# Kernel tuning notes

Measured on AMD Instinct MI355X. Metric: run time of the kernel, lower is better.

The kernel has to match this reference:

```python
import jax, jax.numpy as jnp
import numpy as np

C = 256
H = 4  # hard-coded head count in SA_Layer reshapes
EPS = 1e-5


def _bn(x, gamma, beta):
    # training-mode BatchNorm1d over (batch, length) per channel; x: [b,c,n]
    m = jnp.mean(x, axis=(0, 2), keepdims=True)
    v = jnp.var(x, axis=(0, 2), keepdims=True)
    return gamma[None, :, None] * (x - m) * jax.lax.rsqrt(v + EPS) + beta[None, :, None]


def _conv1(w, x, b=None):
    # 1x1 Conv1d == per-point matmul; w: [o,c], x: [b,c,n]
    y = jnp.einsum('oc,bcn->bon', w, x)
    return y if b is None else y + b[None, :, None]


def _sa_layer(x, xyz_emb, qk_w, v_w, v_b, t_w, t_b, bn_g, bn_b):
    b, c, n = x.shape
    h = x + xyz_emb                      # [b,c,n]
    q = _conv1(qk_w, h)                  # [b,c,n]  (q and k share weights)
    # quirky reshape: permute to [b,n,c] then view as [b,H,n,c//H]
    x_q = jnp.transpose(q, (0, 2, 1)).reshape(b, H, n, c // H)
    x_k = q.reshape(b, H, c // H, n)     # standard channel head split
    x_v = _conv1(v_w, h, v_b).reshape(b, H, c // H, n)
    energy = jnp.matmul(x_q, x_k)        # [b,H,n,n]
    att = jax.nn.softmax(energy, axis=-1)
    att = jax.nn.softmax(att, axis=-2)   # dual softmax
    x_r = jnp.matmul(x_v, att).reshape(b, c, n)
    x_r = jax.nn.relu(_bn(_conv1(t_w, x - x_r, t_b), bn_g, bn_b))
    return x + x_r


def setup_inputs() -> dict:
    key = jax.random.key(0)
    ks = jax.random.split(key, 16)
    B, N = 4, 2048
    s = 1.0 / np.sqrt(C)
    inp = {
        'x': jax.random.normal(ks[0], (B, C, N), jnp.float32),
        'xyz': jax.random.normal(ks[1], (B, N, 3), jnp.float32),
        'conv1_w': jax.random.normal(ks[2], (C, C), jnp.float32) * s,
        'pos_w': jax.random.normal(ks[3], (C, 3), jnp.float32) * 0.5,
        'pos_b': jax.random.normal(ks[4], (C,), jnp.float32) * 0.02,
        'bn1_g': jnp.ones((C,), jnp.float32),
        'bn1_b': jnp.zeros((C,), jnp.float32),
        'qk_w': jax.random.normal(ks[5], (4, C, C), jnp.float32) * s,
        'v_w': jax.random.normal(ks[6], (4, C, C), jnp.float32) * s,
        'v_b': jax.random.normal(ks[7], (4, C), jnp.float32) * 0.02,
        't_w': jax.random.normal(ks[8], (4, C, C), jnp.float32) * s,
        't_b': jax.random.normal(ks[9], (4, C), jnp.float32) * 0.02,
        'bn_g': jnp.ones((4, C), jnp.float32),
        'bn_b': jnp.zeros((4, C), jnp.float32),
    }
    return inp


def reference(x, xyz, conv1_w, pos_w, pos_b, bn1_g, bn1_b,
              qk_w, v_w, v_b, t_w, t_b, bn_g, bn_b):
    # xyz: [B,N,3] -> permute -> pos_xyz (1x1 conv)
    xyz_emb = jnp.einsum('oi,bni->bon', pos_w, xyz) + pos_b[None, :, None]  # [b,C,n]
    h = jax.nn.relu(_bn(_conv1(conv1_w, x), bn1_g, bn1_b))
    outs = []
    for i in range(4):
        h = _sa_layer(h, xyz_emb, qk_w[i], v_w[i], v_b[i],
                      t_w[i], t_b[i], bn_g[i], bn_b[i])
        outs.append(h)
    return jnp.concatenate(outs, axis=1)  # [b, 4*C, n]
```

## Files before the change

### kernel.cpp

```cpp
#include <hip/hip_runtime.h>
#include <math.h>

#define Bsz 4
#define Cch 256
#define Npt 2048
#define Hh  4
#define NL  4
#define BN_CNT (Bsz * Npt)
#define EPSV 1e-5f
#define NROW (16 * Npt)
#define L2E 1.44269504f
#define NIC 4

typedef _Float16 f16x8 __attribute__((ext_vector_type(8)));
typedef _Float16 f16x4 __attribute__((ext_vector_type(4)));
typedef float    f32x4 __attribute__((ext_vector_type(4)));

__device__ __forceinline__ float fexp2(float x) { return __builtin_amdgcn_exp2f(x); }

__device__ __forceinline__ void gld16(const _Float16* g, _Float16* l) {
    __builtin_amdgcn_global_load_lds(
        (const __attribute__((address_space(1))) unsigned int*)g,
        (__attribute__((address_space(3))) unsigned int*)l, 16, 0, 0);
}

__global__ void k_xyz_emb(const float* __restrict__ xyz, const float* __restrict__ pw,
                          const float* __restrict__ pb, float* __restrict__ emb) {
    int idx = blockIdx.x * 256 + threadIdx.x;
    int n = idx & (Npt - 1);
    int c = (idx >> 11) & (Cch - 1);
    int b = idx >> 19;
    const float* xz = xyz + (b * Npt + n) * 3;
    emb[idx] = pw[c * 3 + 0] * xz[0] + pw[c * 3 + 1] * xz[1] + pw[c * 3 + 2] * xz[2] + pb[c];
}

__global__ void k_castw(const float* __restrict__ c1w, const float* __restrict__ qkw,
                        const float* __restrict__ vw, const float* __restrict__ tw,
                        _Float16* __restrict__ o, float* __restrict__ bnacc) {
    int i = blockIdx.x * 256 + threadIdx.x;
    if (i < 5 * 512) bnacc[i] = 0.f;
    const float* src; int off;
    if (i < 65536)            { src = c1w; off = i; }
    else if (i < 327680)      { src = qkw; off = i - 65536; }
    else if (i < 589824)      { src = vw;  off = i - 327680; }
    else                      { src = tw;  off = i - 589824; }
    o[i] = (_Float16)src[off];
}

__global__ __launch_bounds__(256) void k_fuse_t(const float* __restrict__ in,
        _Float16* __restrict__ XT) {
    __shared__ _Float16 Tt[64][72];
    const int b = blockIdx.z, c0 = blockIdx.y * 64, n0 = blockIdx.x * 64;
    const int t = threadIdx.x;
    const int cl = t >> 2, ns = (t & 3) * 16;
    const float* ip = in + ((size_t)(b * Cch + c0 + cl) * Npt) + n0 + ns;
    #pragma unroll
    for (int g = 0; g < 4; ++g) {
        float4 v = *(const float4*)(ip + g * 4);
        Tt[ns + g * 4 + 0][cl] = (_Float16)v.x;
        Tt[ns + g * 4 + 1][cl] = (_Float16)v.y;
        Tt[ns + g * 4 + 2][cl] = (_Float16)v.z;
        Tt[ns + g * 4 + 3][cl] = (_Float16)v.w;
    }
    __syncthreads();
    int nl = t >> 2, cs = (t & 3) * 16;
    _Float16* op = XT + ((size_t)(b * Npt + n0 + nl) * Cch) + c0 + cs;
    #pragma unroll
    for (int g = 0; g < 4; ++g)
        *(f16x4*)(op + g * 4) = *(f16x4*)&Tt[nl][cs + g * 4];
}

__global__ __launch_bounds__(256) void k_gemm_mfma(const _Float16* __restrict__ Wb,
        const _Float16* __restrict__ XT, const float* __restrict__ bias,
        float* __restrict__ Yf, float* __restrict__ bnacc) {
    __shared__ float EpF[64][68];
    const int b = blockIdx.z, o0 = blockIdx.y * 64, n0 = blockIdx.x * 64;
    const int tid = threadIdx.x, w = tid >> 6, quad = (tid >> 4) & 3, tx = tid & 15;
    const _Float16* Arow = Wb + (o0 + w * 16 + tx) * Cch + quad * 8;
    const _Float16* Brow = XT + ((size_t)(b * Npt + n0 + tx) * Cch) + quad * 8;
    f32x4 acc[4];
    #pragma unroll
    for (int s = 0; s < 4; ++s) acc[s] = (f32x4){0.f, 0.f, 0.f, 0.f};
    for (int k0 = 0; k0 < Cch; k0 += 32) {
        f16x8 a = *(const f16x8*)(Arow + k0);
        #pragma unroll
        for (int s = 0; s < 4; ++s) {
            f16x8 bb = *(const f16x8*)(Brow + s * 16 * Cch + k0);
            acc[s] = __builtin_amdgcn_mfma_f32_16x16x32_f16(a, bb, acc[s], 0, 0, 0);
        }
    }
    float bv[4];
    {
        int ob = o0 + w * 16 + quad * 4;
        if (bias) { bv[0] = bias[ob]; bv[1] = bias[ob + 1]; bv[2] = bias[ob + 2]; bv[3] = bias[ob + 3]; }
        else bv[0] = bv[1] = bv[2] = bv[3] = 0.f;
    }
    #pragma unroll
    for (int s = 0; s < 4; ++s) {
        int ol = w * 16 + quad * 4, nl = s * 16 + tx;
        EpF[ol + 0][nl] = acc[s][0] + bv[0];
        EpF[ol + 1][nl] = acc[s][1] + bv[1];
        EpF[ol + 2][nl] = acc[s][2] + bv[2];
        EpF[ol + 3][nl] = acc[s][3] + bv[3];
    }
    __syncthreads();
    int row = tid >> 2, seg = (tid & 3) * 16;
    float* yp = Yf + ((size_t)(b * Cch + o0 + row) * Npt) + n0 + seg;
    float s1 = 0.f, s2 = 0.f;
    #pragma unroll
    for (int g = 0; g < 4; ++g) {
        float4 v = *(float4*)&EpF[row][seg + g * 4];
        *(float4*)(yp + g * 4) = v;
        s1 += v.x + v.y + v.z + v.w;
        s2 += v.x * v.x + v.y * v.y + v.z * v.z + v.w * v.w;
    }
    s1 += __shfl_xor(s1, 1); s2 += __shfl_xor(s2, 1);
    s1 += __shfl_xor(s1, 2); s2 += __shfl_xor(s2, 2);
    if ((tid & 3) == 0) {
        atomicAdd(&bnacc[o0 + row], s1);
        atomicAdd(&bnacc[256 + o0 + row], s2);
    }
}

__global__ __launch_bounds__(256) void k_gemm_qkv(const _Float16* __restrict__ Wqk,
        const _Float16* __restrict__ Wv, const _Float16* __restrict__ XT,
        const float* __restrict__ vbias, _Float16* __restrict__ Vb,
        _Float16* __restrict__ Qg, _Float16* __restrict__ Kt) {
    __shared__ _Float16 EpB[64][72];
    const int b = blockIdx.z, y = blockIdx.y, n0 = blockIdx.x * 64;
    const int isV = (y >= 4);
    const int o0 = (isV ? (y - 4) : y) * 64;
    const _Float16* Wb = isV ? Wv : Wqk;
    const int tid = threadIdx.x, w = tid >> 6, quad = (tid >> 4) & 3, tx = tid & 15;
    const _Float16* Arow = Wb + (o0 + w * 16 + tx) * Cch + quad * 8;
    const _Float16* Brow = XT + ((size_t)(b * Npt + n0 + tx) * Cch) + quad * 8;
    f32x4 acc[4];
    #pragma unroll
    for (int s = 0; s < 4; ++s) acc[s] = (f32x4){0.f, 0.f, 0.f, 0.f};
    for (int k0 = 0; k0 < Cch; k0 += 32) {
        f16x8 a = *(const f16x8*)(Arow + k0);
        #pragma unroll
        for (int s = 0; s < 4; ++s) {
            f16x8 bb = *(const f16x8*)(Brow + s * 16 * Cch + k0);
            acc[s] = __builtin_amdgcn_mfma_f32_16x16x32_f16(a, bb, acc[s], 0, 0, 0);
        }
    }
    if (!isV) {
        const int cch = (w << 1) + (quad >> 1);
        const int hof = (quad & 1) * 4;
        #pragma unroll
        for (int s = 0; s < 4; ++s) {
            int ng = n0 + s * 16 + tx;
            f16x4 pk;
            pk[0] = (_Float16)acc[s][0]; pk[1] = (_Float16)acc[s][1];
            pk[2] = (_Float16)acc[s][2]; pk[3] = (_Float16)acc[s][3];
            int rK = ng & 63, jt = ng >> 6;
            size_t ka = ((size_t)((b * Hh + (o0 >> 6)) * 32 + jt) << 12)
                      + rK * 64 + ((cch ^ (rK & 7)) * 8) + hof;
            *(f16x4*)&Kt[ka] = pk;
            int iQ = ((ng & 511) << 2) + (o0 >> 6);
            int rQ = iQ & 63, it = iQ >> 6;
            size_t qa = ((size_t)((b * Hh + (ng >> 9)) * 32 + it) << 12)
                      + rQ * 64 + ((cch ^ (rQ & 7)) * 8) + hof;
            *(f16x4*)&Qg[qa] = pk;
        }
        return;
    }
    float bv[4];
    {
        int ob = o0 + w * 16 + quad * 4;
        bv[0] = vbias[ob]; bv[1] = vbias[ob + 1]; bv[2] = vbias[ob + 2]; bv[3] = vbias[ob + 3];
    }
    #pragma unroll
    for (int s = 0; s < 4; ++s) {
        int ol = w * 16 + quad * 4, nl = s * 16 + tx;
        EpB[ol + 0][nl] = (_Float16)(acc[s][0] + bv[0]);
        EpB[ol + 1][nl] = (_Float16)(acc[s][1] + bv[1]);
        EpB[ol + 2][nl] = (_Float16)(acc[s][2] + bv[2]);
        EpB[ol + 3][nl] = (_Float16)(acc[s][3] + bv[3]);
    }
    __syncthreads();
    int row = tid >> 2, seg = (tid & 3) * 16;
    _Float16* yp = Vb + ((size_t)(b * Cch + o0 + row) * Npt) + n0 + seg;
    #pragma unroll
    for (int g = 0; g < 4; ++g)
        *(f16x4*)(yp + g * 4) = *(f16x4*)&EpB[row][seg + g * 4];
}

__global__ __launch_bounds__(256) void k_attn_A(const _Float16* __restrict__ Qg,
        const _Float16* __restrict__ Kt, float* __restrict__ mP, float* __restrict__ lP) {
    __shared__ _Float16 Ksh[2][4096];
    const int flat = blockIdx.x;
    const int bh = (flat & 7) * 2 + ((flat >> 3) & 1);
    const int rest = flat >> 4;
    const int i0 = (rest & 15) * 128;
    const int jc = rest >> 4;
    const int tid = threadIdx.x, w = tid >> 6, q = (tid >> 4) & 3, tx = tid & 15;
    const int lane = tid & 63;
    const int sx = tx & 7;
    f16x8 qa[2][2];
    #pragma unroll
    for (int g = 0; g < 2; ++g) {
        const _Float16* Qtile = Qg + ((size_t)(bh * 32 + ((i0 + g * 64) >> 6)) << 12);
        int r = w * 16 + tx;
        qa[g][0] = *(const f16x8*)(Qtile + r * 64 + (q ^ sx) * 8);
        qa[g][1] = *(const f16x8*)(Qtile + r * 64 + ((q + 4) ^ sx) * 8);
    }
    const _Float16* Kbase = Kt + ((size_t)(bh * 32) << 12);
    const int jt0 = jc * 8;
    {
        const _Float16* g = Kbase + ((size_t)jt0 << 12) + (w * 2) * 512 + lane * 8;
        gld16(g,       &Ksh[0][(w * 2 + 0) * 512]);
        gld16(g + 512, &Ksh[0][(w * 2 + 1) * 512]);
    }
    __syncthreads();
    float m2[2][4], l[2][4];
    #pragma unroll
    for (int g = 0; g < 2; ++g)
        #pragma unroll
        for (int r = 0; r < 4; ++r) { m2[g][r] = -1e30f; l[g][r] = 0.f; }
    for (int t = 0; t < 8; ++t) {
        if (t < 7) {
            const _Float16* g = Kbase + ((size_t)(jt0 + t + 1) << 12) + (w * 2) * 512 + lane * 8;
            gld16(g,       &Ksh[(t + 1) & 1][(w * 2 + 0) * 512]);
            gld16(g + 512, &Ksh[(t + 1) & 1][(w * 2 + 1) * 512]);
        }
        const _Float16* kbuf = Ksh[t & 1];
        f32x4 e[2][4];
        #pragma unroll
        for (int s = 0; s < 4; ++s) {
            int r = s * 16 + tx;
            f16x8 kb0 = *(const f16x8*)(kbuf + r * 64 + (q ^ sx) * 8);
            f16x8 kb1 = *(const f16x8*)(kbuf + r * 64 + ((q + 4) ^ sx) * 8);
            #pragma unroll
            for (int g = 0; g < 2; ++g) {
                f32x4 z = (f32x4){0.f, 0.f, 0.f, 0.f};
                z = __builtin_amdgcn_mfma_f32_16x16x32_f16(qa[g][0], kb0, z, 0, 0, 0);
                e[g][s] = __builtin_amdgcn_mfma_f32_16x16x32_f16(qa[g][1], kb1, z, 0, 0, 0);
            }
        }
        #pragma unroll
        for (int g = 0; g < 2; ++g)
            #pragma unroll
            for (int r = 0; r < 4; ++r) {
                float e0 = e[g][0][r] * L2E, e1 = e[g][1][r] * L2E;
                float e2 = e[g][2][r] * L2E, e3 = e[g][3][r] * L2E;
                float lm = fmaxf(fmaxf(e0, e1), fmaxf(e2, e3));
                float nm = fmaxf(m2[g][r], lm);
                l[g][r] = l[g][r] * fexp2(m2[g][r] - nm)
                        + fexp2(e0 - nm) + fexp2(e1 - nm) + fexp2(e2 - nm) + fexp2(e3 - nm);
                m2[g][r] = nm;
            }
        __syncthreads();
    }
    #pragma unroll
    for (int g = 0; g < 2; ++g)
        #pragma unroll
        for (int r = 0; r < 4; ++r) {
            float mm = m2[g][r], ll = l[g][r];
            #pragma unroll
            for (int off = 1; off < 16; off <<= 1) {
                float om = __shfl_xor(mm, off), ol = __shfl_xor(ll, off);
                float nm = fmaxf(mm, om);
                ll = ll * fexp2(mm - nm) + ol * fexp2(om - nm);
                mm = nm;
            }
            if (tx == 0) {
                int idx = bh * Npt + i0 + g * 64 + w * 16 + q * 4 + r;
                mP[jc * NROW + idx] = mm;
                lP[jc * NROW + idx] = ll;
            }
        }
}

__global__ void k_mlcomb(const float* __restrict__ mP, const float* __restrict__ lP,
                         float* __restrict__ rowm2, float* __restrict__ rowli2) {
    int row = blockIdx.x * 256 + threadIdx.x;
    float m0 = mP[row], m1 = mP[NROW + row], m2 = mP[2 * NROW + row], m3 = mP[3 * NROW + row];
    float m = fmaxf(fmaxf(m0, m1), fmaxf(m2, m3));
    float l = lP[row] * fexp2(m0 - m) + lP[NROW + row] * fexp2(m1 - m)
            + lP[2 * NROW + row] * fexp2(m2 - m) + lP[3 * NROW + row] * fexp2(m3 - m);
    rowm2[row] = m;
    rowli2[row] = L2E / l;
}

__global__ __launch_bounds__(256) void k_attn_B(const _Float16* __restrict__ Qg,
        const _Float16* __restrict__ Kt, const _Float16* __restrict__ Vb,
        const float* __restrict__ rowm2, const float* __restrict__ rowli2,
        _Float16* __restrict__ Tp, float* __restrict__ Sp) {
    __shared__ _Float16 AtT[4][4096];
    const int flat = blockIdx.x;
    const int bh = (flat & 7) * 2 + ((flat >> 3) & 1);
    const int j0 = (flat >> 4) * 64;
    const int b = bh >> 2, hd = bh & 3;
    const int tid = threadIdx.x, w = tid >> 6, q = (tid >> 4) & 3, tx = tid & 15;
    const int sx = tx & 7;
    f16x8 kb[4][2];
    const _Float16* Ktile = Kt + ((size_t)(bh * 32 + (j0 >> 6)) << 12);
    #pragma unroll
    for (int nt = 0; nt < 4; ++nt) {
        int r = nt * 16 + tx;
        kb[nt][0] = *(const f16x8*)(Ktile + r * 64 + (q ^ sx) * 8);
        kb[nt][1] = *(const f16x8*)(Ktile + r * 64 + ((q + 4) ^ sx) * 8);
    }
    f32x4 Tacc[4][4];
    #pragma unroll
    for (int mt = 0; mt < 4; ++mt)
        #pragma unroll
        for (int nt = 0; nt < 4; ++nt) Tacc[mt][nt] = (f32x4){0.f, 0.f, 0.f, 0.f};
    float scS[4] = {0.f, 0.f, 0.f, 0.f};
    _Float16* myAt = AtT[w];
    const _Float16* vbase = Vb + (size_t)(b * Cch + hd * 64) * Npt;
    const float* m2b = rowm2 + bh * Npt;
    const float* lib = rowli2 + bh * Npt;
    for (int it = 0; it < 8; ++it) {
        const int i0 = w * 512 + it * 64;
        const _Float16* Qtile = Qg + ((size_t)(bh * 32 + (i0 >> 6)) << 12);
        #pragma unroll
        for (int mt = 0; mt < 4; ++mt) {
            int r = mt * 16 + tx;
            f16x8 qa0 = *(const f16x8*)(Qtile + r * 64 + (q ^ sx) * 8);
            f16x8 qa1 = *(const f16x8*)(Qtile + r * 64 + ((q + 4) ^ sx) * 8);
            float4 m2v = *(const float4*)(m2b + i0 + mt * 16 + q * 4);
            float4 liv = *(const float4*)(lib + i0 + mt * 16 + q * 4);
            #pragma unroll
            for (int nt = 0; nt < 4; ++nt) {
                f32x4 z = (f32x4){0.f, 0.f, 0.f, 0.f};
                z = __builtin_amdgcn_mfma_f32_16x16x32_f16(qa0, kb[nt][0], z, 0, 0, 0);
                z = __builtin_amdgcn_mfma_f32_16x16x32_f16(qa1, kb[nt][1], z, 0, 0, 0);
                float a0 = fexp2(fexp2(__builtin_fmaf(z[0], L2E, -m2v.x)) * liv.x);
                float a1 = fexp2(fexp2(__builtin_fmaf(z[1], L2E, -m2v.y)) * liv.y);
                float a2 = fexp2(fexp2(__builtin_fmaf(z[2], L2E, -m2v.z)) * liv.z);
                float a3 = fexp2(fexp2(__builtin_fmaf(z[3], L2E, -m2v.w)) * liv.w);
                scS[nt] += a0 + a1 + a2 + a3;
                f16x4 pk;
                pk[0] = (_Float16)a0; pk[1] = (_Float16)a1;
                pk[2] = (_Float16)a2; pk[3] = (_Float16)a3;
                *(f16x4*)&myAt[(nt * 16 + tx) * 64 + ((2 * mt + (q >> 1)) ^ sx) * 8 + (q & 1) * 4] = pk;
            }
        }
        f16x8 pb[4][2], va[4][2];
        #pragma unroll
        for (int nt = 0; nt < 4; ++nt) {
            int r = nt * 16 + tx;
            pb[nt][0] = *(const f16x8*)&myAt[r * 64 + (q ^ sx) * 8];
            pb[nt][1] = *(const f16x8*)&myAt[r * 64 + ((q + 4) ^ sx) * 8];
        }
        #pragma unroll
        for (int mt = 0; mt < 4; ++mt) {
            const _Float16* vp = vbase + (size_t)(mt * 16 + tx) * Npt + i0 + q * 8;
            va[mt][0] = *(const f16x8*)(vp);
            va[mt][1] = *(const f16x8*)(vp + 32);
        }
        #pragma unroll
        for (int mt = 0; mt < 4; ++mt)
            #pragma unroll
            for (int nt = 0; nt < 4; ++nt) {
                Tacc[mt][nt] = __builtin_amdgcn_mfma_f32_16x16x32_f16(va[mt][0], pb[nt][0], Tacc[mt][nt], 0, 0, 0);
                Tacc[mt][nt] = __builtin_amdgcn_mfma_f32_16x16x32_f16(va[mt][1], pb[nt][1], Tacc[mt][nt], 0, 0, 0);
            }
    }
    const size_t NE = (size_t)Bsz * Cch * Npt;
    #pragma unroll
    for (int mt = 0; mt < 4; ++mt)
        #pragma unroll
        for (int nt = 0; nt < 4; ++nt) {
            int d = hd * 64 + mt * 16 + q * 4;
            int jg = j0 + nt * 16 + tx;
            _Float16* tp = Tp + (size_t)w * NE + (size_t)(b * Cch + d) * Npt + jg;
            tp[0 * Npt] = (_Float16)Tacc[mt][nt][0];
            tp[1 * Npt] = (_Float16)Tacc[mt][nt][1];
            tp[2 * Npt] = (_Float16)Tacc[mt][nt][2];
            tp[3 * Npt] = (_Float16)Tacc[mt][nt][3];
        }
    #pragma unroll
    for (int nt = 0; nt < 4; ++nt) {
        float s = scS[nt];
        s += __shfl_xor(s, 16);
        s += __shfl_xor(s, 32);
        if (q == 0) Sp[(size_t)w * NROW + bh * Npt + j0 + nt * 16 + tx] = s;
    }
}

__global__ __launch_bounds__(256) void k_redT_fuse(const float* __restrict__ h,
        const _Float16* __restrict__ Tp, const float* __restrict__ Sp,
        _Float16* __restrict__ XT) {
    __shared__ _Float16 Tt[64][72];
    __shared__ float rsL[64];
    const int b = blockIdx.z, c0 = blockIdx.y * 64, n0 = blockIdx.x * 64;
    const int t = threadIdx.x;
    const int bh = b * Hh + (c0 >> 6);
    if (t < 64) {
        float s = 0.f;
        #pragma unroll
        for (int ic = 0; ic < NIC; ++ic) s += Sp[(size_t)ic * NROW + bh * Npt + n0 + t];
        rsL[t] = 1.f / s;
    }
    __syncthreads();
    const int cl = t >> 2, ns = (t & 3) * 16;
    const size_t NE = (size_t)Bsz * Cch * Npt;
    const size_t rowoff = ((size_t)(b * Cch + c0 + cl) * Npt) + n0 + ns;
    float tv[16];
    #pragma unroll
    for (int e = 0; e < 16; ++e) tv[e] = 0.f;
    #pragma unroll
    for (int ic = 0; ic < NIC; ++ic) {
        const _Float16* qq = Tp + (size_t)ic * NE + rowoff;
        #pragma unroll
        for (int g = 0; g < 2; ++g) {
            f16x8 vv = *(const f16x8*)(qq + g * 8);
            #pragma unroll
            for (int e = 0; e < 8; ++e) tv[g * 8 + e] += (float)vv[e];
        }
    }
    const float* hp = h + rowoff;
    #pragma unroll
    for (int g = 0; g < 4; ++g) {
        float4 hv = *(const float4*)(hp + g * 4);
        Tt[ns + g * 4 + 0][cl] = (_Float16)(hv.x - tv[g * 4 + 0] * rsL[ns + g * 4 + 0]);
        Tt[ns + g * 4 + 1][cl] = (_Float16)(hv.y - tv[g * 4 + 1] * rsL[ns + g * 4 + 1]);
        Tt[ns + g * 4 + 2][cl] = (_Float16)(hv.z - tv[g * 4 + 2] * rsL[ns + g * 4 + 2]);
        Tt[ns + g * 4 + 3][cl] = (_Float16)(hv.w - tv[g * 4 + 3] * rsL[ns + g * 4 + 3]);
    }
    __syncthreads();
    int nl = t >> 2, cs = (t & 3) * 16;
    _Float16* op = XT + ((size_t)(b * Npt + n0 + nl) * Cch) + c0 + cs;
    #pragma unroll
    for (int g = 0; g < 4; ++g)
        *(f16x4*)(op + g * 4) = *(f16x4*)&Tt[nl][cs + g * 4];
}

__global__ __launch_bounds__(256) void k_bn_fuse(const float* __restrict__ t,
        const float* __restrict__ bnacc,
        const float* __restrict__ g, const float* __restrict__ bt,
        const float* __restrict__ emb, const float* __restrict__ resid,
        float* __restrict__ hout, float* __restrict__ out, _Float16* __restrict__ XT,
        int layer) {
    __shared__ _Float16 Tt[64][72];
    const int b = blockIdx.z, c0 = blockIdx.y * 64, n0 = blockIdx.x * 64;
    const int tt = threadIdx.x;
    const int cl = tt >> 2, ns = (tt & 3) * 16;
    const int c = c0 + cl;
    const float mn = bnacc[c] * (1.f / BN_CNT);
    const float var = bnacc[256 + c] * (1.f / BN_CNT) - mn * mn;
    const float is = rsqrtf(var + EPSV);
    const float gg = g[c], bb = bt[c];
    const size_t rowoff = ((size_t)(b * Cch + c) * Npt) + n0 + ns;
    const float* tp = t + rowoff;
    const float* ep = emb + rowoff;
    const float* rp = resid ? resid + rowoff : nullptr;
    float* hp = hout + rowoff;
    float* op = out ? out + (size_t)b * (NL * Cch * Npt) + (size_t)(layer * Cch + c) * Npt + n0 + ns
                    : nullptr;
    #pragma unroll
    for (int gi = 0; gi < 4; ++gi) {
        float4 v = *(const float4*)(tp + gi * 4);
        float4 y;
        y.x = fmaxf(gg * (v.x - mn) * is + bb, 0.f);
        y.y = fmaxf(gg * (v.y - mn) * is + bb, 0.f);
        y.z = fmaxf(gg * (v.z - mn) * is + bb, 0.f);
        y.w = fmaxf(gg * (v.w - mn) * is + bb, 0.f);
        if (rp) {
            float4 r = *(const float4*)(rp + gi * 4);
            y.x += r.x; y.y += r.y; y.z += r.z; y.w += r.w;
        }
        *(float4*)(hp + gi * 4) = y;
        if (op) *(float4*)(op + gi * 4) = y;
        float4 e = *(const float4*)(ep + gi * 4);
        Tt[ns + gi * 4 + 0][cl] = (_Float16)(y.x + e.x);
        Tt[ns + gi * 4 + 1][cl] = (_Float16)(y.y + e.y);
        Tt[ns + gi * 4 + 2][cl] = (_Float16)(y.z + e.z);
        Tt[ns + gi * 4 + 3][cl] = (_Float16)(y.w + e.w);
    }
    __syncthreads();
    int nl = tt >> 2, cs = (tt & 3) * 16;
    _Float16* xp = XT + ((size_t)(b * Npt + n0 + nl) * Cch) + c0 + cs;
    #pragma unroll
    for (int gi = 0; gi < 4; ++gi)
        *(f16x4*)(xp + gi * 4) = *(f16x4*)&Tt[nl][cs + gi * 4];
}

extern "C" void kernel_launch(void* const* d_in, const int* in_sizes, int n_in,
                              void* d_out, int out_size, void* d_ws, size_t ws_size,
                              hipStream_t stream) {
    (void)in_sizes; (void)n_in; (void)out_size; (void)ws_size;
    const float* x    = (const float*)d_in[0];
    const float* xyz  = (const float*)d_in[1];
    const float* c1w  = (const float*)d_in[2];
    const float* posw = (const float*)d_in[3];
    const float* posb = (const float*)d_in[4];
    const float* bn1g = (const float*)d_in[5];
    const float* bn1b = (const float*)d_in[6];
    const float* qkw  = (const float*)d_in[7];
    const float* vw   = (const float*)d_in[8];
    const float* vb   = (const float*)d_in[9];
    const float* tw   = (const float*)d_in[10];
    const float* tb   = (const float*)d_in[11];
    const float* bng  = (const float*)d_in[12];
    const float* bnb  = (const float*)d_in[13];
    float* out = (float*)d_out;

    const size_t NE = (size_t)Bsz * Cch * Npt;
    char* W = (char*)d_ws;
    float* emb   = (float*)W;                 W += NE * 4;
    float* h     = (float*)W;                 W += NE * 4;
    float* vbuf  = (float*)W;                 W += NE * 4;
    _Float16* Tp = (_Float16*)W;              W += (size_t)NIC * NE * 2;
    _Float16* XT = (_Float16*)W;              W += NE * 2;
    _Float16* Qg = (_Float16*)W;              W += NE * 2;
    _Float16* Kt = (_Float16*)W;              W += NE * 2;
    _Float16* Vb = (_Float16*)W;              W += NE * 2;
    _Float16* wbf = (_Float16*)W;             W += 851968 * 2;
    float* rowm2 = (float*)W;                 W += NROW * 4;
    float* rowli2 = (float*)W;                W += NROW * 4;
    float* mP    = (float*)W;                 W += 4 * NROW * 4;
    float* lP    = (float*)W;                 W += 4 * NROW * 4;
    float* Sp    = (float*)W;                 W += NIC * NROW * 4;
    float* bnacc = (float*)W;                 W += 5 * 512 * 4;

    dim3 blk(256);
    dim3 g4(Npt / 64, Cch / 64, Bsz);
    dim3 gQKV(Npt / 64, 8, Bsz);
    int ew = (int)(NE / 256);

    k_castw<<<3328, blk, 0, stream>>>(c1w, qkw, vw, tw, wbf, bnacc);
    k_xyz_emb<<<ew, blk, 0, stream>>>(xyz, posw, posb, emb);

    k_fuse_t<<<g4, blk, 0, stream>>>(x, XT);
    k_gemm_mfma<<<g4, blk, 0, stream>>>(wbf, XT, nullptr, vbuf, bnacc);
    k_bn_fuse<<<g4, blk, 0, stream>>>(vbuf, bnacc, bn1g, bn1b, emb, nullptr,
                                      h, nullptr, XT, 0);

    for (int L = 0; L < NL; ++L) {
        const _Float16* qkL = wbf + 65536 + (size_t)L * 65536;
        const _Float16* vL  = wbf + 327680 + (size_t)L * 65536;
        const _Float16* tL  = wbf + 589824 + (size_t)L * 65536;
        float* accL = bnacc + (1 + L) * 512;
        k_gemm_qkv<<<gQKV, blk, 0, stream>>>(qkL, vL, XT, vb + L * Cch, Vb, Qg, Kt);
        k_attn_A<<<1024, blk, 0, stream>>>(Qg, Kt, mP, lP);
        k_mlcomb<<<NROW / 256, blk, 0, stream>>>(mP, lP, rowm2, rowli2);
        k_attn_B<<<512, blk, 0, stream>>>(Qg, Kt, Vb, rowm2, rowli2, Tp, Sp);
        k_redT_fuse<<<g4, blk, 0, stream>>>(h, Tp, Sp, XT);
        k_gemm_mfma<<<g4, blk, 0, stream>>>(tL, XT, tb + L * Cch, vbuf, accL);
        k_bn_fuse<<<g4, blk, 0, stream>>>(vbuf, accL, bng + L * Cch, bnb + L * Cch,
                                          emb, h, h, out, XT, L);
    }
}
```

Baseline: 624.8 us.

## Fuse row-stat combine and partial-T reduction into attention B kernel

Each attention-B block now combines the per-chunk softmax max/sum statistics for its head into LDS itself, replacing the separate combine kernel. The per-wave partial T accumulators are summed through shared memory and the residual subtract and transpose to XT are done in-kernel, removing the Tp/Sp global buffers and the separate reduction kernel. This cuts large fp16 global round-trips and launches, at the cost of redundant stat recomputation per block and higher LDS use that may lower occupancy.

```diff
diff --git a/kernel.cpp b/kernel.cpp
--- a/kernel.cpp
+++ b/kernel.cpp
@@ -10,7 +10,6 @@
 #define EPSV 1e-5f
 #define NROW (16 * Npt)
 #define L2E 1.44269504f
-#define NIC 4
 
 typedef _Float16 f16x8 __attribute__((ext_vector_type(8)));
 typedef _Float16 f16x4 __attribute__((ext_vector_type(4)));
@@ -273,28 +272,51 @@
         }
 }
 
-__global__ void k_mlcomb(const float* __restrict__ mP, const float* __restrict__ lP,
-                         float* __restrict__ rowm2, float* __restrict__ rowli2) {
-    int row = blockIdx.x * 256 + threadIdx.x;
-    float m0 = mP[row], m1 = mP[NROW + row], m2 = mP[2 * NROW + row], m3 = mP[3 * NROW + row];
-    float m = fmaxf(fmaxf(m0, m1), fmaxf(m2, m3));
-    float l = lP[row] * fexp2(m0 - m) + lP[NROW + row] * fexp2(m1 - m)
-            + lP[2 * NROW + row] * fexp2(m2 - m) + lP[3 * NROW + row] * fexp2(m3 - m);
-    rowm2[row] = m;
-    rowli2[row] = L2E / l;
-}
-
 __global__ __launch_bounds__(256) void k_attn_B(const _Float16* __restrict__ Qg,
         const _Float16* __restrict__ Kt, const _Float16* __restrict__ Vb,
-        const float* __restrict__ rowm2, const float* __restrict__ rowli2,
-        _Float16* __restrict__ Tp, float* __restrict__ Sp) {
+        const float* __restrict__ mP, const float* __restrict__ lP,
+        const float* __restrict__ h, _Float16* __restrict__ XT) {
     __shared__ _Float16 AtT[4][4096];
+    __shared__ float mlm[Npt];
+    __shared__ float mll[Npt];
+    __shared__ float Ssh[4][64];
+    __shared__ float rsv[64];
+    __shared__ _Float16 Tt[64][72];
     const int flat = blockIdx.x;
     const int bh = (flat & 7) * 2 + ((flat >> 3) & 1);
     const int j0 = (flat >> 4) * 64;
     const int b = bh >> 2, hd = bh & 3;
     const int tid = threadIdx.x, w = tid >> 6, q = (tid >> 4) & 3, tx = tid & 15;
     const int sx = tx & 7;
+    {
+        const int ib = tid * 8;
+        #pragma unroll
+        for (int e = 0; e < 2; ++e) {
+            int ii = ib + e * 4;
+            int idx = bh * Npt + ii;
+            float4 m0 = *(const float4*)&mP[idx];
+            float4 m1 = *(const float4*)&mP[NROW + idx];
+            float4 m2 = *(const float4*)&mP[2 * NROW + idx];
+            float4 m3 = *(const float4*)&mP[3 * NROW + idx];
+            float4 l0 = *(const float4*)&lP[idx];
+            float4 l1 = *(const float4*)&lP[NROW + idx];
+            float4 l2 = *(const float4*)&lP[2 * NROW + idx];
+            float4 l3 = *(const float4*)&lP[3 * NROW + idx];
+            #pragma unroll
+            for (int k = 0; k < 4; ++k) {
+                float a0 = ((const float*)&m0)[k], a1 = ((const float*)&m1)[k];
+                float a2 = ((const float*)&m2)[k], a3 = ((const float*)&m3)[k];
+                float mm = fmaxf(fmaxf(a0, a1), fmaxf(a2, a3));
+                float ll = ((const float*)&l0)[k] * fexp2(a0 - mm)
+                         + ((const float*)&l1)[k] * fexp2(a1 - mm)
+                         + ((const float*)&l2)[k] * fexp2(a2 - mm)
+                         + ((const float*)&l3)[k] * fexp2(a3 - mm);
+                mlm[ii + k] = mm;
+                mll[ii + k] = L2E / ll;
+            }
+        }
+    }
+    __syncthreads();
     f16x8 kb[4][2];
     const _Float16* Ktile = Kt + ((size_t)(bh * 32 + (j0 >> 6)) << 12);
     #pragma unroll
@@ -311,8 +333,6 @@
     float scS[4] = {0.f, 0.f, 0.f, 0.f};
     _Float16* myAt = AtT[w];
     const _Float16* vbase = Vb + (size_t)(b * Cch + hd * 64) * Npt;
-    const float* m2b = rowm2 + bh * Npt;
-    const float* lib = rowli2 + bh * Npt;
     for (int it = 0; it < 8; ++it) {
         const int i0 = w * 512 + it * 64;
         const _Float16* Qtile = Qg + ((size_t)(bh * 32 + (i0 >> 6)) << 12);
@@ -321,8 +341,8 @@
             int r = mt * 16 + tx;
             f16x8 qa0 = *(const f16x8*)(Qtile + r * 64 + (q ^ sx) * 8);
             f16x8 qa1 = *(const f16x8*)(Qtile + r * 64 + ((q + 4) ^ sx) * 8);
-            float4 m2v = *(const float4*)(m2b + i0 + mt * 16 + q * 4);
-            float4 liv = *(const float4*)(lib + i0 + mt * 16 + q * 4);
+            float4 m2v = *(const float4*)&mlm[i0 + mt * 16 + q * 4];
+            float4 liv = *(const float4*)&mll[i0 + mt * 16 + q * 4];
             #pragma unroll
             for (int nt = 0; nt < 4; ++nt) {
                 f32x4 z = (f32x4){0.f, 0.f, 0.f, 0.f};
@@ -360,74 +380,52 @@
                 Tacc[mt][nt] = __builtin_amdgcn_mfma_f32_16x16x32_f16(va[mt][1], pb[nt][1], Tacc[mt][nt], 0, 0, 0);
             }
     }
-    const size_t NE = (size_t)Bsz * Cch * Npt;
     #pragma unroll
     for (int mt = 0; mt < 4; ++mt)
         #pragma unroll
         for (int nt = 0; nt < 4; ++nt) {
-            int d = hd * 64 + mt * 16 + q * 4;
-            int jg = j0 + nt * 16 + tx;
-            _Float16* tp = Tp + (size_t)w * NE + (size_t)(b * Cch + d) * Npt + jg;
-            tp[0 * Npt] = (_Float16)Tacc[mt][nt][0];
-            tp[1 * Npt] = (_Float16)Tacc[mt][nt][1];
-            tp[2 * Npt] = (_Float16)Tacc[mt][nt][2];
-            tp[3 * Npt] = (_Float16)Tacc[mt][nt][3];
+            f16x4 pk;
+            pk[0] = (_Float16)Tacc[mt][nt][0];
+            pk[1] = (_Float16)Tacc[mt][nt][1];
+            pk[2] = (_Float16)Tacc[mt][nt][2];
+            pk[3] = (_Float16)Tacc[mt][nt][3];
+            *(f16x4*)&myAt[(nt * 16 + tx) * 64 + mt * 16 + q * 4] = pk;
         }
     #pragma unroll
     for (int nt = 0; nt < 4; ++nt) {
         float s = scS[nt];
         s += __shfl_xor(s, 16);
         s += __shfl_xor(s, 32);
-        if (q == 0) Sp[(size_t)w * NROW + bh * Npt + j0 + nt * 16 + tx] = s;
-    }
-}
-
-__global__ __launch_bounds__(256) void k_redT_fuse(const float* __restrict__ h,
-        const _Float16* __restrict__ Tp, const float* __restrict__ Sp,
-        _Float16* __restrict__ XT) {
-    __shared__ _Float16 Tt[64][72];
-    __shared__ float rsL[64];
-    const int b = blockIdx.z, c0 = blockIdx.y * 64, n0 = blockIdx.x * 64;
-    const int t = threadIdx.x;
-    const int bh = b * Hh + (c0 >> 6);
-    if (t < 64) {
-        float s = 0.f;
-        #pragma unroll
-        for (int ic = 0; ic < NIC; ++ic) s += Sp[(size_t)ic * NROW + bh * Npt + n0 + t];
-        rsL[t] = 1.f / s;
-    }
-    __syncthreads();
-    const int cl = t >> 2, ns = (t & 3) * 16;
-    const size_t NE = (size_t)Bsz * Cch * Npt;
-    const size_t rowoff = ((size_t)(b * Cch + c0 + cl) * Npt) + n0 + ns;
-    float tv[16];
-    #pragma unroll
-    for (int e = 0; e < 16; ++e) tv[e] = 0.f;
-    #pragma unroll
-    for (int ic = 0; ic < NIC; ++ic) {
-        const _Float16* qq = Tp + (size_t)ic * NE + rowoff;
-        #pragma unroll
-        for (int g = 0; g < 2; ++g) {
-            f16x8 vv = *(const f16x8*)(qq + g * 8);
-            #pragma unroll
-            for (int e = 0; e < 8; ++e) tv[g * 8 + e] += (float)vv[e];
-        }
-    }
-    const float* hp = h + rowoff;
-    #pragma unroll
-    for (int g = 0; g < 4; ++g) {
-        float4 hv = *(const float4*)(hp + g * 4);
-        Tt[ns + g * 4 + 0][cl] = (_Float16)(hv.x - tv[g * 4 + 0] * rsL[ns + g * 4 + 0]);
-        Tt[ns + g * 4 + 1][cl] = (_Float16)(hv.y - tv[g * 4 + 1] * rsL[ns + g * 4 + 1]);
-        Tt[ns + g * 4 + 2][cl] = (_Float16)(hv.z - tv[g * 4 + 2] * rsL[ns + g * 4 + 2]);
-        Tt[ns + g * 4 + 3][cl] = (_Float16)(hv.w - tv[g * 4 + 3] * rsL[ns + g * 4 + 3]);
-    }
-    __syncthreads();
-    int nl = t >> 2, cs = (t & 3) * 16;
-    _Float16* op = XT + ((size_t)(b * Npt + n0 + nl) * Cch) + c0 + cs;
-    #pragma unroll
-    for (int g = 0; g < 4; ++g)
-        *(f16x4*)(op + g * 4) = *(f16x4*)&Tt[nl][cs + g * 4];
+        if (q == 0) Ssh[w][nt * 16 + tx] = s;
+    }
+    __syncthreads();
+    if (tid < 64)
+        rsv[tid] = 1.f / (Ssh[0][tid] + Ssh[1][tid] + Ssh[2][tid] + Ssh[3][tid]);
+    __syncthreads();
+    {
+        const int cl = tid >> 2, ns = (tid & 3) * 16;
+        const float* hp = h + ((size_t)(b * Cch + hd * 64 + cl) * Npt) + j0 + ns;
+        #pragma unroll
+        for (int g = 0; g < 4; ++g) {
+            float4 hv = *(const float4*)(hp + g * 4);
+            #pragma unroll
+            for (int k = 0; k < 4; ++k) {
+                int jl = ns + g * 4 + k;
+                float tv = (float)AtT[0][jl * 64 + cl] + (float)AtT[1][jl * 64 + cl]
+                         + (float)AtT[2][jl * 64 + cl] + (float)AtT[3][jl * 64 + cl];
+                float hvk = ((const float*)&hv)[k];
+                Tt[jl][cl] = (_Float16)(hvk - tv * rsv[jl]);
+            }
+        }
+    }
+    __syncthreads();
+    {
+        int nl = tid >> 2, cs = (tid & 3) * 16;
+        _Float16* op = XT + ((size_t)(b * Npt + j0 + nl) * Cch) + hd * 64 + cs;
+        #pragma unroll
+        for (int g = 0; g < 4; ++g)
+            *(f16x4*)(op + g * 4) = *(f16x4*)&Tt[nl][cs + g * 4];
+    }
 }
 
 __global__ __launch_bounds__(256) void k_bn_fuse(const float* __restrict__ t,
@@ -505,17 +503,13 @@
     float* emb   = (float*)W;                 W += NE * 4;
     float* h     = (float*)W;                 W += NE * 4;
     float* vbuf  = (float*)W;                 W += NE * 4;
-    _Float16* Tp = (_Float16*)W;              W += (size_t)NIC * NE * 2;
     _Float16* XT = (_Float16*)W;              W += NE * 2;
     _Float16* Qg = (_Float16*)W;              W += NE * 2;
     _Float16* Kt = (_Float16*)W;              W += NE * 2;
     _Float16* Vb = (_Float16*)W;              W += NE * 2;
     _Float16* wbf = (_Float16*)W;             W += 851968 * 2;
-    float* rowm2 = (float*)W;                 W += NROW * 4;
-    float* rowli2 = (float*)W;                W += NROW * 4;
     float* mP    = (float*)W;                 W += 4 * NROW * 4;
     float* lP    = (float*)W;                 W += 4 * NROW * 4;
-    float* Sp    = (float*)W;                 W += NIC * NROW * 4;
     float* bnacc = (float*)W;                 W += 5 * 512 * 4;
 
     dim3 blk(256);
@@ -538,9 +532,7 @@
         float* accL = bnacc + (1 + L) * 512;
         k_gemm_qkv<<<gQKV, blk, 0, stream>>>(qkL, vL, XT, vb + L * Cch, Vb, Qg, Kt);
         k_attn_A<<<1024, blk, 0, stream>>>(Qg, Kt, mP, lP);
-        k_mlcomb<<<NROW / 256, blk, 0, stream>>>(mP, lP, rowm2, rowli2);
-        k_attn_B<<<512, blk, 0, stream>>>(Qg, Kt, Vb, rowm2, rowli2, Tp, Sp);
-        k_redT_fuse<<<g4, blk, 0, stream>>>(h, Tp, Sp, XT);
+        k_attn_B<<<512, blk, 0, stream>>>(Qg, Kt, Vb, mP, lP, h, XT);
         k_gemm_mfma<<<g4, blk, 0, stream>>>(tL, XT, tb + L * Cch, vbuf, accL);
         k_bn_fuse<<<g4, blk, 0, stream>>>(vbuf, accL, bng + L * Cch, bnb + L * Cch,
                                           emb, h, h, out, XT, L);
```

Result: faster. 603.4 us (-3.4%).
